# Performance work log

Measured on AMD Instinct MI355X. Metric: run time of the kernel, lower is better.

## Reference

```python
import jax, jax.numpy as jnp
import numpy as np

S, B, E = 2048, 2, 1024
H = 16
HD = E // H
RANK = 8
ALPHA = 16.0
LORA_SCALE = ALPHA / RANK


def setup_inputs() -> dict:
    key = jax.random.key(0)
    ks = jax.random.split(key, 13)
    d = {
        'query': jax.random.normal(ks[0], (S, B, E), jnp.float32),
        'key': jax.random.normal(ks[1], (S, B, E), jnp.float32),
        'value': jax.random.normal(ks[2], (S, B, E), jnp.float32),
        'in_proj_weight': jax.random.normal(ks[3], (3 * E, E), jnp.float32) * 0.02,
        'in_proj_bias': jax.random.normal(ks[4], (3 * E,), jnp.float32) * 0.02,
        'out_w': jax.random.normal(ks[5], (E, E), jnp.float32) * 0.02,
        'out_b': jax.random.normal(ks[6], (E,), jnp.float32) * 0.02,
        'A_q': jax.random.normal(ks[7], (RANK, E), jnp.float32) * 0.02,
        'B_q': jax.random.normal(ks[8], (E, RANK), jnp.float32) * 0.02,
        'A_k': jax.random.normal(ks[9], (RANK, E), jnp.float32) * 0.02,
        'B_k': jax.random.normal(ks[10], (E, RANK), jnp.float32) * 0.02,
        'A_v': jax.random.normal(ks[11], (RANK, E), jnp.float32) * 0.02,
        'B_v': jax.random.normal(ks[12], (E, RANK), jnp.float32) * 0.02,
    }
    return d


def _proj(x, W, b, A, Bm):
    # frozen linear + LoRA low-rank delta: x @ W.T + b + ((x @ A.T) @ B.T) * scale
    base = jnp.einsum('sbe,fe->sbf', x, W) + b
    lora = jnp.einsum('sbr,fr->sbf', jnp.einsum('sbe,re->sbr', x, A), Bm) * LORA_SCALE
    return base + lora


def reference(query, key, value, in_proj_weight, in_proj_bias, out_w, out_b,
              A_q, B_q, A_k, B_k, A_v, B_v):
    Wq, Wk, Wv = in_proj_weight[:E], in_proj_weight[E:2 * E], in_proj_weight[2 * E:]
    bq, bk, bv = in_proj_bias[:E], in_proj_bias[E:2 * E], in_proj_bias[2 * E:]
    q = _proj(query, Wq, bq, A_q, B_q)   # [S,B,E]
    k = _proj(key, Wk, bk, A_k, B_k)
    v = _proj(value, Wv, bv, A_v, B_v)
    # reshape to [B*H, S, HD] (seq-first layout, matching torch view/transpose)
    def heads(x):
        return x.reshape(S, B * H, HD).transpose(1, 0, 2)
    qh, kh, vh = heads(q), heads(k), heads(v)
    scale = HD ** -0.5
    attn = jnp.einsum('nsd,ntd->nst', qh, kh) * scale  # [B*H,S,S]
    attn = jax.nn.softmax(attn, axis=-1)
    out = jnp.einsum('nst,ntd->nsd', attn, vh)         # [B*H,S,HD]
    out = out.transpose(1, 0, 2).reshape(S, B, E)
    out = jnp.einsum('sbe,fe->sbf', out, out_w) + out_b
    return out
```

## Files before the change

### kernel.cpp

```cpp
#include <hip/hip_runtime.h>
#include <stdint.h>

static const int S_ = 2048, B_ = 2, E_ = 1024, H_ = 16, HD_ = 64, MR_ = 4096;

typedef __bf16 bf16;
typedef __bf16 bf16x8 __attribute__((ext_vector_type(8)));
typedef float  f32x4  __attribute__((ext_vector_type(4)));
typedef float  f32x16 __attribute__((ext_vector_type(16)));
typedef unsigned short u16x8 __attribute__((ext_vector_type(8)));
typedef short  s16x4  __attribute__((ext_vector_type(4)));

#define AS1(p) ((const __attribute__((address_space(1))) void*)(p))
#define AS3(p) ((__attribute__((address_space(3))) void*)(p))

#define QSCALE 0.18033688011112042f

static __device__ __forceinline__ uint32_t cvtpk_bf16(float lo, float hi) {
    uint32_t r;
    asm("v_cvt_pk_bf16_f32 %0, %1, %2" : "=v"(r) : "v"(lo), "v"(hi));
    return r;
}

__global__ __launch_bounds__(256) void cvt_all(const float* __restrict__ s0,
                                               const float* __restrict__ s1,
                                               const float* __restrict__ s2,
                                               const float* __restrict__ s3,
                                               bf16* __restrict__ d0,
                                               bf16* __restrict__ d1,
                                               bf16* __restrict__ d2,
                                               bf16* __restrict__ d3) {
    int b = blockIdx.x;
    const float* src;
    bf16* dst;
    int i;
    if (b < 6144) {
        int seg = b >> 11;
        i = (b & 2047) * 256 + threadIdx.x;
        src = seg == 0 ? s0 : (seg == 1 ? s1 : s2);
        dst = seg == 0 ? d0 : (seg == 1 ? d1 : d2);
    } else {
        i = (b - 6144) * 256 + threadIdx.x;
        src = s3; dst = d3;
    }
    const float4* s = (const float4*)src;
    float4 a = s[i * 2], c = s[i * 2 + 1];
    bf16x8 v;
    v[0] = (bf16)a.x; v[1] = (bf16)a.y; v[2] = (bf16)a.z; v[3] = (bf16)a.w;
    v[4] = (bf16)c.x; v[5] = (bf16)c.y; v[6] = (bf16)c.z; v[7] = (bf16)c.w;
    *(bf16x8*)(dst + (size_t)i * 8) = v;
}

__global__ __launch_bounds__(256) void build_weff3(const float* __restrict__ W,
                                                   const float* __restrict__ A0,
                                                   const float* __restrict__ B0,
                                                   const float* __restrict__ A1,
                                                   const float* __restrict__ B1,
                                                   const float* __restrict__ A2,
                                                   const float* __restrict__ B2,
                                                   bf16* __restrict__ o0,
                                                   bf16* __restrict__ o1,
                                                   bf16* __restrict__ o2) {
    int z = blockIdx.y;
    const float* A = z == 0 ? A0 : (z == 1 ? A1 : A2);
    const float* Bm = z == 0 ? B0 : (z == 1 ? B1 : B2);
    bf16* out = z == 0 ? o0 : (z == 1 ? o1 : o2);
    const float* Wz = W + (size_t)z * 1024 * 1024;
    int idx = blockIdx.x * 256 + threadIdx.x;
    int f = idx >> 10, e = idx & 1023;
    float acc = Wz[idx];
#pragma unroll
    for (int r = 0; r < 8; r++) acc += 2.0f * Bm[f * 8 + r] * A[r * 1024 + e];
    out[idx] = (bf16)acc;
}

__global__ __launch_bounds__(256) void gemm_qkv(const bf16* __restrict__ XQ,
                                                const bf16* __restrict__ XK,
                                                const bf16* __restrict__ XV,
                                                const bf16* __restrict__ WQ,
                                                const bf16* __restrict__ WK,
                                                const bf16* __restrict__ WV,
                                                const float* __restrict__ ipb,
                                                bf16* __restrict__ QH,
                                                bf16* __restrict__ KH,
                                                bf16* __restrict__ VH) {
    int z = blockIdx.z;
    const bf16* Amat = z == 0 ? XQ : (z == 1 ? XK : XV);
    const bf16* Bmat = z == 0 ? WQ : (z == 1 ? WK : WV);
    bf16* Cout = z == 0 ? QH : (z == 1 ? KH : VH);
    const float* bias = ipb + z * 1024;
    float cscale = z == 0 ? QSCALE : 1.0f;

    __shared__ bf16 smbuf[16896];
    const int tid = threadIdx.x;
    const int wid = tid >> 6, lane = tid & 63;
    const int lg = lane >> 4, li = lane & 15;
    const int m0 = blockIdx.y * 128, n0 = blockIdx.x * 128;
    const int wr = wid >> 1, wc = wid & 1;

    f32x4 acc[4][4] = {};

    for (int kt = 0; kt < 1024; kt += 64) {
        __syncthreads();
#pragma unroll
        for (int h = 0; h < 2; h++)
#pragma unroll
            for (int i = 0; i < 2; i++) {
                int c = wid * 2 + i;
                const bf16* ga = Amat + (size_t)(m0 + c * 16 + (lane >> 2)) * 1024 + kt + h * 32 + (lane & 3) * 8;
                __builtin_amdgcn_global_load_lds(AS1(ga), AS3(smbuf + h * 4096 + c * 512), 16, 0, 0);
                const bf16* gb = Bmat + (size_t)(n0 + c * 16 + (lane >> 2)) * 1024 + kt + h * 32 + (lane & 3) * 8;
                __builtin_amdgcn_global_load_lds(AS1(gb), AS3(smbuf + 8192 + h * 4096 + c * 512), 16, 0, 0);
            }
        __syncthreads();

#pragma unroll
        for (int h = 0; h < 2; h++) {
            bf16x8 a[4], b[4];
#pragma unroll
            for (int mi = 0; mi < 4; mi++)
                a[mi] = *(const bf16x8*)(smbuf + h * 4096 + (wr * 64 + mi * 16 + li) * 32 + lg * 8);
#pragma unroll
            for (int ni = 0; ni < 4; ni++)
                b[ni] = *(const bf16x8*)(smbuf + 8192 + h * 4096 + (wc * 64 + ni * 16 + li) * 32 + lg * 8);
#pragma unroll
            for (int mi = 0; mi < 4; mi++)
#pragma unroll
                for (int ni = 0; ni < 4; ni++)
                    acc[mi][ni] = __builtin_amdgcn_mfma_f32_16x16x32_bf16(a[mi], b[ni], acc[mi][ni], 0, 0, 0);
        }
    }

    __syncthreads();
#pragma unroll
    for (int ni = 0; ni < 4; ni++) {
        int fl = wc * 64 + ni * 16 + li;
        float bv = bias[n0 + fl];
#pragma unroll
        for (int mi = 0; mi < 4; mi++)
#pragma unroll
            for (int r = 0; r < 4; r++) {
                int ml_ = wr * 64 + mi * 16 + lg * 4 + r;
                smbuf[ml_ * 132 + fl] = (bf16)((acc[mi][ni][r] + bv) * cscale);
            }
    }
    __syncthreads();
#pragma unroll
    for (int k = 0; k < 8; k++) {
        int c = tid + 256 * k;
        int dhalf = c & 7, m = (c >> 3) & 127, hl = c >> 10;
        u16x8 v = *(const u16x8*)(smbuf + m * 132 + hl * 64 + dhalf * 8);
        int mg = m0 + m, fg = n0 + hl * 64;
        int s = mg >> 1, bb = mg & 1, h = fg >> 6, d = dhalf * 8;
        *(u16x8*)(Cout + (size_t)(bb * 16 + h) * S_ * 64 + (size_t)s * 64 + d) = v;
    }
}

__global__ __launch_bounds__(256) void gemm_out64(const bf16* __restrict__ Amat,
                                                  const bf16* __restrict__ Bmat,
                                                  const float* __restrict__ bias,
                                                  float* __restrict__ Cout) {
    __shared__ bf16 Asm[2][64 * 32];
    __shared__ bf16 Bsm[2][128 * 32];
    const int tid = threadIdx.x;
    const int wid = tid >> 6, lane = tid & 63;
    const int lg = lane >> 4, li = lane & 15;
    const int m0 = blockIdx.y * 64, n0 = blockIdx.x * 128;
    const int wr = wid >> 1, wc = wid & 1;

    f32x4 acc[2][4] = {};

    for (int kt = 0; kt < 1024; kt += 64) {
        __syncthreads();
#pragma unroll
        for (int h = 0; h < 2; h++)
            for (int j = wid; j < 12; j += 4) {
                if (j < 4) {
                    const bf16* ga = Amat + (size_t)(m0 + j * 16 + (lane >> 2)) * 1024 + kt + h * 32 + (lane & 3) * 8;
                    __builtin_amdgcn_global_load_lds(AS1(ga), AS3(&Asm[h][j * 512]), 16, 0, 0);
                } else {
                    int c = j - 4;
                    const bf16* gb = Bmat + (size_t)(n0 + c * 16 + (lane >> 2)) * 1024 + kt + h * 32 + (lane & 3) * 8;
                    __builtin_amdgcn_global_load_lds(AS1(gb), AS3(&Bsm[h][c * 512]), 16, 0, 0);
                }
            }
        __syncthreads();

#pragma unroll
        for (int h = 0; h < 2; h++) {
            bf16x8 a[2], b[4];
#pragma unroll
            for (int mi = 0; mi < 2; mi++)
                a[mi] = *(const bf16x8*)(&Asm[h][(wr * 32 + mi * 16 + li) * 32 + lg * 8]);
#pragma unroll
            for (int ni = 0; ni < 4; ni++)
                b[ni] = *(const bf16x8*)(&Bsm[h][(wc * 64 + ni * 16 + li) * 32 + lg * 8]);
#pragma unroll
            for (int mi = 0; mi < 2; mi++)
#pragma unroll
                for (int ni = 0; ni < 4; ni++)
                    acc[mi][ni] = __builtin_amdgcn_mfma_f32_16x16x32_bf16(a[mi], b[ni], acc[mi][ni], 0, 0, 0);
        }
    }

#pragma unroll
    for (int ni = 0; ni < 4; ni++) {
        int f = n0 + wc * 64 + ni * 16 + li;
        float bv = bias[f];
#pragma unroll
        for (int mi = 0; mi < 2; mi++)
#pragma unroll
            for (int r = 0; r < 4; r++) {
                int m = m0 + wr * 32 + mi * 16 + lg * 4 + r;
                Cout[(size_t)m * 1024 + f] = acc[mi][ni][r] + bv;
            }
    }
}

__global__ __launch_bounds__(256, 4) void attn_fwd(const bf16* __restrict__ qh,
                                                   const bf16* __restrict__ kh,
                                                   const bf16* __restrict__ vh,
                                                   bf16* __restrict__ outbuf) {
    __shared__ __attribute__((aligned(16))) char smem[33280];

    const int bid = blockIdx.x;
    const int head = (bid & 7) * 4 + ((bid >> 3) & 3);
    const int qt = bid >> 5;
    const int tid = threadIdx.x, wid = tid >> 6, l = tid & 63;
    const int li = l & 31, hi = l >> 5;
    const int kvh = wid & 1;

    const bf16* Qb = qh + (size_t)head * S_ * 64;
    const bf16* Kb = kh + (size_t)head * S_ * 64;
    const bf16* Vb = vh + (size_t)head * S_ * 64;
    const int q0 = qt * 64 + (wid >> 1) * 32;

    bf16x8 qf[4];
#pragma unroll
    for (int s = 0; s < 4; s++)
        qf[s] = *(const bf16x8*)(Qb + (size_t)(q0 + li) * 64 + 16 * s + 8 * hi);

    f32x16 oacc0 = {}, oacc1 = {};
    float lsum = 0.f;

    const size_t kg_off = ((size_t)(16 * (l & 7)) ^ (16 * ((l >> 3) & 7)));
    const int vk2 = tid & 31, vdb = (tid >> 5) * 8;
    const int rswz = 16 * (li & 7);
    const int vswz = 8 * (li & 15);

#define STAGE_K(kv0, dstbuf)                                                    \
    {                                                                           \
        _Pragma("unroll")                                                       \
        for (int j = 0; j < 2; j++) {                                           \
            int row = (j * 4 + wid) * 8 + (l >> 3);                             \
            const char* srcp = (const char*)Kb + (size_t)((kv0) + row) * 128 + kg_off; \
            __builtin_amdgcn_global_load_lds(AS1(srcp),                         \
                AS3((dstbuf) + (j * 4 + wid) * 1024), 16, 0, 0);                \
        }                                                                       \
    }

    u16x8 vreg0, vreg1;
    vreg0 = *(const u16x8*)(Vb + (size_t)(2 * vk2) * 64 + vdb);
    vreg1 = *(const u16x8*)(Vb + (size_t)(2 * vk2 + 1) * 64 + vdb);
    STAGE_K(0, smem);

    for (int t = 0; t < 32; t++) {
        const int cur = t & 1;
        char* Kc = smem + cur * 8192;
        char* Vc = smem + 16384 + cur * 8192;
#pragma unroll
        for (int i = 0; i < 8; i++) {
            uint32_t w = (uint32_t)vreg0[i] | ((uint32_t)vreg1[i] << 16);
            *(uint32_t*)(Vc + (vdb + i) * 128 + ((4 * vk2) ^ (8 * ((vdb + i) & 15)))) = w;
        }
        __syncthreads();
        if (t + 1 < 32) {
            int kv0 = (t + 1) * 64;
            vreg0 = *(const u16x8*)(Vb + (size_t)(kv0 + 2 * vk2) * 64 + vdb);
            vreg1 = *(const u16x8*)(Vb + (size_t)(kv0 + 2 * vk2 + 1) * 64 + vdb);
            STAGE_K(kv0, smem + (cur ^ 1) * 8192);
        }

        f32x16 s = {};
        __builtin_amdgcn_s_setprio(1);
#pragma unroll
        for (int step = 0; step < 4; step++) {
            bf16x8 k0 = *(const bf16x8*)(Kc + (kvh * 32 + li) * 128 + ((32 * step + 16 * hi) ^ rswz));
            s = __builtin_amdgcn_mfma_f32_32x32x16_bf16(k0, qf[step], s, 0, 0, 0);
        }
        __builtin_amdgcn_s_setprio(0);

        float p[16];
#pragma unroll
        for (int r = 0; r < 16; r++) {
            p[r] = __builtin_amdgcn_exp2f(s[r]);
            lsum += p[r];
        }
        s16x4 pa[4];
#pragma unroll
        for (int st = 0; st < 4; st++) {
            uint32_t w0 = cvtpk_bf16(p[4 * st], p[4 * st + 1]);
            uint32_t w1 = cvtpk_bf16(p[4 * st + 2], p[4 * st + 3]);
            union { uint32_t u[2]; s16x4 v; } pu;
            pu.u[0] = w0; pu.u[1] = w1;
            pa[st] = pu.v;
        }

        __builtin_amdgcn_s_setprio(1);
#pragma unroll
        for (int st = 0; st < 4; st++) {
            int byteoff = (64 * kvh + 16 * st + 8 * hi) ^ vswz;
            s16x4 v0 = *(const s16x4*)(Vc + li * 128 + byteoff);
            s16x4 v1 = *(const s16x4*)(Vc + (32 + li) * 128 + byteoff);
            asm("v_mfma_f32_32x32x8_bf16 %0, %1, %2, %0"
                : "+v"(oacc0) : "v"(pa[st]), "v"(v0));
            asm("v_mfma_f32_32x32x8_bf16 %0, %1, %2, %0"
                : "+v"(oacc1) : "v"(pa[st]), "v"(v1));
        }
        __builtin_amdgcn_s_setprio(0);
    }

    __syncthreads();
    float* mlp = (float*)(smem + 32768);
    float* scr = (float*)smem;
    float lt = lsum + __shfl_xor(lsum, 32);
    if (l < 32) mlp[wid * 32 + l] = lt;
    {
        float* mys = scr + wid * 1024;
#pragma unroll
        for (int r = 0; r < 16; r++) {
            int rp = (r & 3) + 8 * (r >> 2) + 4 * hi;
            mys[rp * 32 + li] = kvh ? oacc0[r] : oacc1[r];
        }
    }
    __syncthreads();
    float pl = mlp[(wid ^ 1) * 32 + li];
    float linv = 1.0f / (lt + pl);
    const float* ps = scr + (wid ^ 1) * 1024;
    int bb = head >> 4, h = head & 15;
#pragma unroll
    for (int r = 0; r < 16; r++) {
        int rp = (r & 3) + 8 * (r >> 2) + 4 * hi;
        int q = q0 + rp;
        float own = kvh ? oacc1[r] : oacc0[r];
        float part = ps[rp * 32 + li];
        float val = (own + part) * __shfl(linv, rp);
        outbuf[(size_t)(q * 2 + bb) * 1024 + h * 64 + kvh * 32 + li] = (bf16)val;
    }
}

extern "C" void kernel_launch(void* const* d_in, const int* in_sizes, int n_in,
                              void* d_out, int out_size, void* d_ws, size_t ws_size,
                              hipStream_t stream) {
    const float* query = (const float*)d_in[0];
    const float* key_  = (const float*)d_in[1];
    const float* value = (const float*)d_in[2];
    const float* ipw   = (const float*)d_in[3];
    const float* ipb   = (const float*)d_in[4];
    const float* out_w = (const float*)d_in[5];
    const float* out_b = (const float*)d_in[6];
    const float* A_q   = (const float*)d_in[7];
    const float* B_q   = (const float*)d_in[8];
    const float* A_k   = (const float*)d_in[9];
    const float* B_k   = (const float*)d_in[10];
    const float* A_v   = (const float*)d_in[11];
    const float* B_v   = (const float*)d_in[12];

    const size_t MB = 1ull << 20;
    if (ws_size < 64 * MB) return;
    char* ws = (char*)d_ws;
    bf16* XQ = (bf16*)(ws + 0 * MB);
    bf16* XK = (bf16*)(ws + 8 * MB);
    bf16* XV = (bf16*)(ws + 16 * MB);
    bf16* WQ = (bf16*)(ws + 24 * MB);
    bf16* WK = (bf16*)(ws + 26 * MB);
    bf16* WV = (bf16*)(ws + 28 * MB);
    bf16* WO = (bf16*)(ws + 30 * MB);
    bf16* QH = (bf16*)(ws + 32 * MB);
    bf16* KH = (bf16*)(ws + 40 * MB);
    bf16* VH = (bf16*)(ws + 48 * MB);
    bf16* AT = (bf16*)(ws + 56 * MB);

    cvt_all<<<6656, 256, 0, stream>>>(query, key_, value, out_w, XQ, XK, XV, WO);
    build_weff3<<<dim3(4096, 3), 256, 0, stream>>>(ipw, A_q, B_q, A_k, B_k, A_v, B_v,
                                                   WQ, WK, WV);

    gemm_qkv<<<dim3(8, 32, 3), 256, 0, stream>>>(XQ, XK, XV, WQ, WK, WV, ipb, QH, KH, VH);

    attn_fwd<<<1024, 256, 0, stream>>>(QH, KH, VH, AT);

    gemm_out64<<<dim3(8, 64), 256, 0, stream>>>(AT, WO, out_b, (float*)d_out);
}
```

Before: 140.1 us.

## Use 32x32x16 MFMA for PV with permlane32 swap, remap GEMM block order

The attention PV product now uses the wider 32x32x16 bf16 MFMA instead of pairs of 32x32x8 instructions. The P fragments are rearranged across lanes with v_permlane32_swap so they match the new operand layout, and the V shared-memory swizzle is changed so each lane can read 16-byte fragments. The row sum is computed as a tree reduction. Both projection GEMMs also remap block indices into an interleaved order to improve L2 reuse of shared A/B tiles. The risk is that the permlane operand mapping or the swizzle change is wrong, which would give incorrect results or LDS bank conflicts.

```diff
diff --git a/kernel.cpp b/kernel.cpp
--- a/kernel.cpp
+++ b/kernel.cpp
@@ -8,7 +8,6 @@
 typedef float  f32x4  __attribute__((ext_vector_type(4)));
 typedef float  f32x16 __attribute__((ext_vector_type(16)));
 typedef unsigned short u16x8 __attribute__((ext_vector_type(8)));
-typedef short  s16x4  __attribute__((ext_vector_type(4)));
 
 #define AS1(p) ((const __attribute__((address_space(1))) void*)(p))
 #define AS3(p) ((__attribute__((address_space(3))) void*)(p))
@@ -94,7 +93,9 @@
     const int tid = threadIdx.x;
     const int wid = tid >> 6, lane = tid & 63;
     const int lg = lane >> 4, li = lane & 15;
-    const int m0 = blockIdx.y * 128, n0 = blockIdx.x * 128;
+    const int bidl = blockIdx.y * 8 + blockIdx.x;
+    const int orig = (bidl & 7) * 32 + (bidl >> 3);
+    const int m0 = (orig >> 3) * 128, n0 = (orig & 7) * 128;
     const int wr = wid >> 1, wc = wid & 1;
 
     f32x4 acc[4][4] = {};
@@ -164,7 +165,9 @@
     const int tid = threadIdx.x;
     const int wid = tid >> 6, lane = tid & 63;
     const int lg = lane >> 4, li = lane & 15;
-    const int m0 = blockIdx.y * 64, n0 = blockIdx.x * 128;
+    const int bidl = blockIdx.y * 8 + blockIdx.x;
+    const int orig = (bidl & 7) * 64 + (bidl >> 3);
+    const int m0 = (orig >> 3) * 64, n0 = (orig & 7) * 128;
     const int wr = wid >> 1, wc = wid & 1;
 
     f32x4 acc[2][4] = {};
@@ -245,7 +248,6 @@
     const size_t kg_off = ((size_t)(16 * (l & 7)) ^ (16 * ((l >> 3) & 7)));
     const int vk2 = tid & 31, vdb = (tid >> 5) * 8;
     const int rswz = 16 * (li & 7);
-    const int vswz = 8 * (li & 15);
 
 #define STAGE_K(kv0, dstbuf)                                                    \
     {                                                                           \
@@ -270,7 +272,7 @@
 #pragma unroll
         for (int i = 0; i < 8; i++) {
             uint32_t w = (uint32_t)vreg0[i] | ((uint32_t)vreg1[i] << 16);
-            *(uint32_t*)(Vc + (vdb + i) * 128 + ((4 * vk2) ^ (8 * ((vdb + i) & 15)))) = w;
+            *(uint32_t*)(Vc + (vdb + i) * 128 + ((4 * vk2) ^ (16 * i))) = w;
         }
         __syncthreads();
         if (t + 1 < 32) {
@@ -291,30 +293,32 @@
 
         float p[16];
 #pragma unroll
-        for (int r = 0; r < 16; r++) {
-            p[r] = __builtin_amdgcn_exp2f(s[r]);
-            lsum += p[r];
-        }
-        s16x4 pa[4];
-#pragma unroll
-        for (int st = 0; st < 4; st++) {
-            uint32_t w0 = cvtpk_bf16(p[4 * st], p[4 * st + 1]);
-            uint32_t w1 = cvtpk_bf16(p[4 * st + 2], p[4 * st + 3]);
-            union { uint32_t u[2]; s16x4 v; } pu;
-            pu.u[0] = w0; pu.u[1] = w1;
+        for (int r = 0; r < 16; r++) p[r] = __builtin_amdgcn_exp2f(s[r]);
+        lsum += (((p[0] + p[1]) + (p[2] + p[3])) + ((p[4] + p[5]) + (p[6] + p[7]))) +
+                (((p[8] + p[9]) + (p[10] + p[11])) + ((p[12] + p[13]) + (p[14] + p[15])));
+
+        bf16x8 pa[2];
+#pragma unroll
+        for (int st = 0; st < 2; st++) {
+            uint32_t a0 = cvtpk_bf16(p[8 * st + 0], p[8 * st + 1]);
+            uint32_t a1 = cvtpk_bf16(p[8 * st + 2], p[8 * st + 3]);
+            uint32_t b0 = cvtpk_bf16(p[8 * st + 4], p[8 * st + 5]);
+            uint32_t b1 = cvtpk_bf16(p[8 * st + 6], p[8 * st + 7]);
+            asm("v_permlane32_swap_b32 %0, %1" : "+v"(a0), "+v"(b0));
+            asm("v_permlane32_swap_b32 %0, %1" : "+v"(a1), "+v"(b1));
+            union { uint32_t u[4]; bf16x8 v; } pu;
+            pu.u[0] = a0; pu.u[1] = a1; pu.u[2] = b0; pu.u[3] = b1;
             pa[st] = pu.v;
         }
 
         __builtin_amdgcn_s_setprio(1);
 #pragma unroll
-        for (int st = 0; st < 4; st++) {
-            int byteoff = (64 * kvh + 16 * st + 8 * hi) ^ vswz;
-            s16x4 v0 = *(const s16x4*)(Vc + li * 128 + byteoff);
-            s16x4 v1 = *(const s16x4*)(Vc + (32 + li) * 128 + byteoff);
-            asm("v_mfma_f32_32x32x8_bf16 %0, %1, %2, %0"
-                : "+v"(oacc0) : "v"(pa[st]), "v"(v0));
-            asm("v_mfma_f32_32x32x8_bf16 %0, %1, %2, %0"
-                : "+v"(oacc1) : "v"(pa[st]), "v"(v1));
+        for (int st = 0; st < 2; st++) {
+            int byteoff = (64 * kvh + 32 * st + 16 * hi) ^ rswz;
+            bf16x8 v0 = *(const bf16x8*)(Vc + li * 128 + byteoff);
+            oacc0 = __builtin_amdgcn_mfma_f32_32x32x16_bf16(pa[st], v0, oacc0, 0, 0, 0);
+            bf16x8 v1 = *(const bf16x8*)(Vc + (32 + li) * 128 + byteoff);
+            oacc1 = __builtin_amdgcn_mfma_f32_32x32x16_bf16(pa[st], v1, oacc1, 0, 0, 0);
         }
         __builtin_amdgcn_s_setprio(0);
     }
```

Result: faster. 129.1 us (-7.9%).
